# Kernel tuning notes

Hardware: AMD Instinct MI355X
Metric: run time of the kernel (lower is better)

The kernel has to match this reference:

```python
import jax, jax.numpy as jnp
import numpy as np

TOPK = 2
NUM_EXPERTS = 8

def setup_inputs() -> dict:
    key = jax.random.key(0)
    kx, kg, k1, k3, k2 = jax.random.split(key, 5)
    B, S, D, F, E = 1, 2048, 1024, 1024, NUM_EXPERTS
    x = jax.random.normal(kx, (B, S, D), dtype=jnp.float32)
    wg = jax.random.normal(kg, (E, D), dtype=jnp.float32) * (1.0 / np.sqrt(D))
    w1 = jax.random.normal(k1, (E, D, F), dtype=jnp.float32) * (1.0 / np.sqrt(D))
    w3 = jax.random.normal(k3, (E, D, F), dtype=jnp.float32) * (1.0 / np.sqrt(D))
    w2 = jax.random.normal(k2, (E, F, D), dtype=jnp.float32) * (1.0 / np.sqrt(F))
    return {"x": x, "wg": wg, "w1": w1, "w3": w3, "w2": w2}

def reference(x, wg, w1, w3, w2):
    # x: [B, S, D] -> tokens [N, D]
    D = x.shape[-1]
    E = wg.shape[0]
    xt = x.reshape(-1, D)
    # Gating: Linear(no bias) + softmax over experts
    logits = xt @ wg.T                      # [N, E]
    gates = jax.nn.softmax(logits, axis=-1)
    # Top-k selection, normalize weights (normalize_expert_weights=True),
    # routed_scaling_factor = 1.0
    weights, idx = jax.lax.top_k(gates, TOPK)      # [N, k]
    weights = weights / weights.sum(axis=-1, keepdims=True)
    # Per-token per-expert combine weight (dispatch+combine equivalent)
    comb = (jax.nn.one_hot(idx, E, dtype=xt.dtype) * weights[..., None]).sum(axis=1)  # [N, E]
    # SwiGLU experts (grouped GEMM equivalent, dense over experts)
    h = jnp.einsum('nd,edf->enf', xt, w1)   # gate proj
    u = jnp.einsum('nd,edf->enf', xt, w3)   # up proj
    a = jax.nn.silu(h) * u                  # [E, N, F]
    out = jnp.einsum('enf,efd,ne->nd', a, w2, comb)
    return out.reshape(x.shape), logits
```

## Files before the change

### kernel.cpp

```cpp
#include <hip/hip_runtime.h>
#include <stdint.h>

typedef unsigned short u16;
typedef __attribute__((ext_vector_type(8))) __bf16 bf16x8;
typedef __attribute__((ext_vector_type(4))) float f32x4;

#define MAXMT 40
#define N_TOK 2048
#define DDIM 1024
#define FDIM 1024

#define DEV static __device__ __forceinline__

DEV float bf2f(u16 u) {
    union { uint32_t i; float f; } v;
    v.i = ((uint32_t)u) << 16;
    return v.f;
}
DEV u16 f2bf(float f) {
    union { float f; uint32_t i; } v;
    v.f = f;
    uint32_t x = v.i;
    return (u16)((x + 0x7fffu + ((x >> 16) & 1u)) >> 16);
}

DEV void async_copy16(const u16* gsrc, u16* ldst) {
    __builtin_amdgcn_global_load_lds(
        (const __attribute__((address_space(1))) void*)(uintptr_t)gsrc,
        (__attribute__((address_space(3))) void*)(uint32_t)(uintptr_t)ldst,
        16, 0, 0);
}

DEV int sniff_fp(const void* p, int tid, int* scnt) {
    if (tid == 0) *scnt = 0;
    __syncthreads();
    u16 u = ((const u16*)p)[tid & 255];
    int e = (u >> 7) & 0xff;
    if (e != 0 && (e < 90 || e > 160)) atomicAdd(scnt, 1);
    __syncthreads();
    return *scnt > 64;
}

__global__ void k_mega(const void* __restrict__ x, const void* __restrict__ wg,
                       const void* __restrict__ w1, const void* __restrict__ w3,
                       const void* __restrict__ w2, u16* __restrict__ wt,
                       u16* __restrict__ xb, void* __restrict__ out_base,
                       int* __restrict__ te, float* __restrict__ tw) {
    __shared__ int scnt;
    __shared__ __align__(16) u16 s[64][72];
    int z = blockIdx.z, tid = threadIdx.x;

    if (z < 24) {
        int which = z >> 3, mat = z & 7;
        const void* src0 = which == 0 ? w1 : (which == 1 ? w3 : w2);
        int fp = sniff_fp(src0, tid, &scnt);
        u16* dst = wt + ((size_t)z) * 1048576;
        int r = tid >> 2, seg = tid & 3;
        int r0 = blockIdx.y * 64, c0 = blockIdx.x * 64;
        size_t base = (size_t)mat * 1048576 + (size_t)(r0 + r) * 1024 + c0 + seg * 16;
        u16 v[16];
        if (fp) {
            const float* sp = (const float*)src0 + base;
#pragma unroll
            for (int q = 0; q < 4; q++) {
                float4 f = ((const float4*)sp)[q];
                v[q * 4 + 0] = f2bf(f.x); v[q * 4 + 1] = f2bf(f.y);
                v[q * 4 + 2] = f2bf(f.z); v[q * 4 + 3] = f2bf(f.w);
            }
        } else {
            const u16* sp = (const u16*)src0 + base;
            *(uint4*)&v[0] = *(const uint4*)sp;
            *(uint4*)&v[8] = *(const uint4*)(sp + 8);
        }
        *(uint4*)&s[r][seg * 16] = *(const uint4*)&v[0];
        *(uint4*)&s[r][seg * 16 + 8] = *(const uint4*)&v[8];
        __syncthreads();
        int col = tid & 63, rgrp = tid >> 6;
        u16 tmp[16];
#pragma unroll
        for (int j = 0; j < 16; j++) tmp[j] = s[rgrp * 16 + j][col];
        u16* dp = dst + (size_t)(c0 + col) * 1024 + r0 + rgrp * 16;
        *(uint4*)dp = *(const uint4*)&tmp[0];
        *(uint4*)(dp + 8) = *(const uint4*)&tmp[8];
    } else {
        int fp = sniff_fp(x, tid, &scnt);
        int gi = (z - 24) * 256 + blockIdx.y * 16 + blockIdx.x;
        int wave = tid >> 6, lane = tid & 63;
        int n = gi * 4 + wave;
        float acc[8];
#pragma unroll
        for (int e = 0; e < 8; e++) acc[e] = 0.f;
        if (fp) {
            const float* xp = (const float*)x + (size_t)n * DDIM;
            const float* wp = (const float*)wg;
            for (int it = 0; it < 16; ++it) {
                int d = it * 64 + lane;
                float xv = xp[d];
                xb[(size_t)n * DDIM + d] = f2bf(xv);
#pragma unroll
                for (int e = 0; e < 8; e++) acc[e] += xv * wp[e * DDIM + d];
            }
        } else {
            const u16* xp = (const u16*)x + (size_t)n * DDIM;
            const u16* wp = (const u16*)wg;
            for (int it = 0; it < 16; ++it) {
                int d = it * 64 + lane;
                u16 raw = xp[d];
                xb[(size_t)n * DDIM + d] = raw;
                float xv = bf2f(raw);
#pragma unroll
                for (int e = 0; e < 8; e++) acc[e] += xv * bf2f(wp[e * DDIM + d]);
            }
        }
#pragma unroll
        for (int e = 0; e < 8; e++) {
            for (int off = 32; off; off >>= 1) acc[e] += __shfl_xor(acc[e], off);
        }
        if (lane < 8) {
            if (fp) ((float*)out_base + (size_t)N_TOK * DDIM)[n * 8 + lane] = acc[lane];
            else    ((u16*)out_base + (size_t)N_TOK * DDIM)[n * 8 + lane] = f2bf(acc[lane]);
        }
        if (lane == 0) {
            int e0 = 0; float b0 = acc[0];
            for (int e = 1; e < 8; e++) if (acc[e] > b0) { b0 = acc[e]; e0 = e; }
            int e1 = -1; float b1 = -1e30f;
            for (int e = 0; e < 8; e++) if (e != e0 && acc[e] > b1) { b1 = acc[e]; e1 = e; }
            float m = fmaxf(b0, b1);
            float x0 = __expf(b0 - m), x1 = __expf(b1 - m);
            float sden = x0 + x1;
            te[n * 2] = e0; te[n * 2 + 1] = e1;
            tw[n * 2] = x0 / sden; tw[n * 2 + 1] = x1 / sden;
        }
    }
}

__global__ void k_sched(const int* __restrict__ te, const float* __restrict__ tw,
                        int* __restrict__ pair_token, float* __restrict__ pair_weight,
                        int* __restrict__ sched) {
    __shared__ int cnt[8], cur[8];
    int t = threadIdx.x;
    if (t < 8) cnt[t] = 0;
    __syncthreads();
    for (int n = t; n < N_TOK; n += 256) {
        atomicAdd(&cnt[te[2 * n]], 1);
        atomicAdd(&cnt[te[2 * n + 1]], 1);
    }
    __syncthreads();
    if (t == 0) {
        int o = 0, mt = 0;
        for (int e = 0; e < 8; e++) {
            cur[e] = o;
            int c = cnt[e];
            for (int m0 = 0; m0 < c; m0 += 128) {
                sched[mt] = e;
                sched[MAXMT + mt] = o + m0;
                sched[2 * MAXMT + mt] = (c - m0 < 128) ? (c - m0) : 128;
                mt++;
            }
            o += c;
        }
        sched[3 * MAXMT] = mt;
        for (int i = mt; i < MAXMT; i++) { sched[i] = 0; sched[MAXMT + i] = 0; sched[2 * MAXMT + i] = 0; }
    }
    __syncthreads();
    for (int n = t; n < N_TOK; n += 256) {
#pragma unroll
        for (int s = 0; s < 2; s++) {
            int e = te[2 * n + s];
            int p = atomicAdd(&cur[e], 1);
            pair_token[p] = n;
            pair_weight[p] = tw[2 * n + s];
        }
    }
}

__launch_bounds__(256, 3)
__global__ void k_gemm13(const u16* __restrict__ xb, const u16* __restrict__ w1t,
                         const u16* __restrict__ w3t, const int* __restrict__ pair_token,
                         const int* __restrict__ sched, u16* __restrict__ Abuf) {
    __shared__ __align__(16) u16 smem[16384];
    u16* sA  = smem;
    u16* sB1 = smem + 8192;
    u16* sB3 = smem + 12288;

    int bn = blockIdx.x;
    int bm = blockIdx.y;
    int total = sched[3 * MAXMT];
    if (bm >= total) return;
    int e = sched[bm];
    int row0 = sched[MAXMT + bm];
    int rowsv = sched[2 * MAXMT + bm];

    int tid = threadIdx.x;
    int wave = tid >> 6, lane = tid & 63;
    int wm = wave & 1, wn = wave >> 1;
    int quad = lane >> 4, l15 = lane & 15;
    int lsub = lane >> 3, slot = lane & 7;

    const u16* gA[4]; u16* lA[4];
#pragma unroll
    for (int c = 0; c < 4; c++) {
        int row = c * 32 + wave * 8 + lsub;
        int cr = row < rowsv ? row : 0;
        int tok = pair_token[row0 + cr];
        int gch = slot ^ (row & 7);
        gA[c] = xb + (size_t)tok * DDIM + gch * 8;
        lA[c] = sA + c * 2048 + wave * 512;
    }
    const u16* gB1[2]; const u16* gB3[2]; int lBoff[2];
#pragma unroll
    for (int c = 0; c < 2; c++) {
        int row = c * 32 + wave * 8 + lsub;
        int gch = slot ^ (row & 7);
        int fcol = bn * 64 + row;
        gB1[c] = w1t + ((size_t)e * 1024 + fcol) * 1024 + gch * 8;
        gB3[c] = w3t + ((size_t)e * 1024 + fcol) * 1024 + gch * 8;
        lBoff[c] = c * 2048 + wave * 512;
    }

    f32x4 acc_h[4][2], acc_u[4][2];
#pragma unroll
    for (int i = 0; i < 4; i++)
#pragma unroll
        for (int j = 0; j < 2; j++) { acc_h[i][j] = (f32x4)0.f; acc_u[i][j] = (f32x4)0.f; }

    for (int kt = 0; kt < 16; ++kt) {
        int k0 = kt * 64;
        __syncthreads();
#pragma unroll
        for (int c = 0; c < 4; c++) async_copy16(gA[c] + k0, lA[c]);
#pragma unroll
        for (int c = 0; c < 2; c++) {
            async_copy16(gB1[c] + k0, sB1 + lBoff[c]);
            async_copy16(gB3[c] + k0, sB3 + lBoff[c]);
        }
        __syncthreads();
#pragma unroll
        for (int kk = 0; kk < 2; ++kk) {
            bf16x8 a[4], b1[2], b3[2];
#pragma unroll
            for (int i = 0; i < 4; i++) {
                int m = wm * 64 + i * 16 + l15;
                int s = (kk * 4 + quad) ^ (m & 7);
                a[i] = *(const bf16x8*)&sA[m * 64 + s * 8];
            }
#pragma unroll
            for (int j = 0; j < 2; j++) {
                int nn = wn * 32 + j * 16 + l15;
                int s = (kk * 4 + quad) ^ (nn & 7);
                b1[j] = *(const bf16x8*)&sB1[nn * 64 + s * 8];
                b3[j] = *(const bf16x8*)&sB3[nn * 64 + s * 8];
            }
#pragma unroll
            for (int i = 0; i < 4; i++)
#pragma unroll
                for (int j = 0; j < 2; j++) {
                    acc_h[i][j] = __builtin_amdgcn_mfma_f32_16x16x32_bf16(a[i], b1[j], acc_h[i][j], 0, 0, 0);
                    acc_u[i][j] = __builtin_amdgcn_mfma_f32_16x16x32_bf16(a[i], b3[j], acc_u[i][j], 0, 0, 0);
                }
        }
    }
    __syncthreads();
#pragma unroll
    for (int i = 0; i < 4; i++)
#pragma unroll
        for (int j = 0; j < 2; j++)
#pragma unroll
            for (int r = 0; r < 4; r++) {
                int row = wm * 64 + i * 16 + quad * 4 + r;
                int col = wn * 32 + j * 16 + l15;
                float h = acc_h[i][j][r], u = acc_u[i][j][r];
                smem[row * 72 + col] = f2bf(h * u / (1.0f + __expf(-h)));
            }
    __syncthreads();
    int rt = tid >> 1, half = tid & 1;
    if (rt < rowsv) {
        u16* dp = Abuf + (size_t)(row0 + rt) * FDIM + bn * 64 + half * 32;
        const u16* sp = &smem[rt * 72 + half * 32];
#pragma unroll
        for (int q = 0; q < 4; q++)
            *(uint4*)(dp + q * 8) = *(const uint4*)(sp + q * 8);
    }
}

__launch_bounds__(256, 3)
__global__ void k_gemm2(const u16* __restrict__ Abuf, const u16* __restrict__ w2t,
                        const int* __restrict__ pair_token, const float* __restrict__ pair_weight,
                        const int* __restrict__ sched, float* __restrict__ outf) {
    __shared__ __align__(16) u16 smem[12288];
    u16* sA = smem;
    u16* sB = smem + 8192;

    int bn = blockIdx.x;
    int bm = blockIdx.y;
    int total = sched[3 * MAXMT];
    if (bm >= total) return;
    int e = sched[bm];
    int row0 = sched[MAXMT + bm];
    int rowsv = sched[2 * MAXMT + bm];

    int tid = threadIdx.x;
    int wave = tid >> 6, lane = tid & 63;
    int wm = wave & 1, wn = wave >> 1;
    int quad = lane >> 4, l15 = lane & 15;
    int lsub = lane >> 3, slot = lane & 7;

    const u16* gA[4]; u16* lA[4];
#pragma unroll
    for (int c = 0; c < 4; c++) {
        int row = c * 32 + wave * 8 + lsub;
        int cr = row < rowsv ? row : 0;
        int gch = slot ^ (row & 7);
        gA[c] = Abuf + (size_t)(row0 + cr) * FDIM + gch * 8;
        lA[c] = sA + c * 2048 + wave * 512;
    }
    const u16* gB[2]; u16* lB[2];
#pragma unroll
    for (int c = 0; c < 2; c++) {
        int row = c * 32 + wave * 8 + lsub;
        int gch = slot ^ (row & 7);
        int dcol = bn * 64 + row;
        gB[c] = w2t + ((size_t)e * 1024 + dcol) * 1024 + gch * 8;
        lB[c] = sB + c * 2048 + wave * 512;
    }

    f32x4 acc[4][2];
#pragma unroll
    for (int i = 0; i < 4; i++)
#pragma unroll
        for (int j = 0; j < 2; j++) acc[i][j] = (f32x4)0.f;

    for (int kt = 0; kt < 16; ++kt) {
        int k0 = kt * 64;
        __syncthreads();
#pragma unroll
        for (int c = 0; c < 4; c++) async_copy16(gA[c] + k0, lA[c]);
#pragma unroll
        for (int c = 0; c < 2; c++) async_copy16(gB[c] + k0, lB[c]);
        __syncthreads();
#pragma unroll
        for (int kk = 0; kk < 2; ++kk) {
            bf16x8 a[4], b[2];
#pragma unroll
            for (int i = 0; i < 4; i++) {
                int m = wm * 64 + i * 16 + l15;
                int s = (kk * 4 + quad) ^ (m & 7);
                a[i] = *(const bf16x8*)&sA[m * 64 + s * 8];
            }
#pragma unroll
            for (int j = 0; j < 2; j++) {
                int nn = wn * 32 + j * 16 + l15;
                int s = (kk * 4 + quad) ^ (nn & 7);
                b[j] = *(const bf16x8*)&sB[nn * 64 + s * 8];
            }
#pragma unroll
            for (int i = 0; i < 4; i++)
#pragma unroll
                for (int j = 0; j < 2; j++)
                    acc[i][j] = __builtin_amdgcn_mfma_f32_16x16x32_bf16(a[i], b[j], acc[i][j], 0, 0, 0);
        }
    }
#pragma unroll
    for (int i = 0; i < 4; i++)
#pragma unroll
        for (int r = 0; r < 4; r++) {
            int lr = wm * 64 + i * 16 + quad * 4 + r;
            if (lr < rowsv) {
                int p = row0 + lr;
                int tok = pair_token[p];
                float w = pair_weight[p];
                float* op = outf + (size_t)tok * DDIM + bn * 64 + wn * 32 + l15;
#pragma unroll
                for (int j = 0; j < 2; j++)
                    atomicAdd(op + j * 16, w * acc[i][j][r]);
            }
        }
}

extern "C" void kernel_launch(void* const* d_in, const int* in_sizes, int n_in,
                              void* d_out, int out_size, void* d_ws, size_t ws_size,
                              hipStream_t stream) {
    const void* x  = d_in[0];
    const void* wg = d_in[1];
    const void* w1 = d_in[2];
    const void* w3 = d_in[3];
    const void* w2 = d_in[4];

    u16* wt   = (u16*)d_ws;
    u16* w1t  = wt;
    u16* w3t  = wt + (size_t)8 * 1048576;
    u16* w2t  = wt + (size_t)16 * 1048576;
    u16* Abuf = wt + (size_t)24 * 1048576;
    u16* xb   = Abuf + (size_t)4096 * 1024;
    int*   te   = (int*)(xb + (size_t)N_TOK * DDIM);
    float* tw   = (float*)(te + 2 * N_TOK);
    int*   ptok = (int*)(tw + 2 * N_TOK);
    float* pwt  = (float*)(ptok + 2 * N_TOK);
    int*   sched = (int*)(pwt + 2 * N_TOK);

    hipMemsetAsync(d_out, 0, (size_t)N_TOK * DDIM * sizeof(float), stream);
    k_mega<<<dim3(16, 16, 26), 256, 0, stream>>>(x, wg, w1, w3, w2, wt, xb, d_out, te, tw);
    k_sched<<<1, 256, 0, stream>>>(te, tw, ptok, pwt, sched);
    k_gemm13<<<dim3(16, MAXMT), 256, 0, stream>>>(xb, w1t, w3t, ptok, sched, Abuf);
    k_gemm2<<<dim3(16, MAXMT), 256, 0, stream>>>(Abuf, w2t, ptok, pwt, sched, (float*)d_out);
}
```

Before: 216.0 us.

## Enlarge transpose tiles, fold output zeroing into mega kernel, pad LDS

```diff
diff --git a/kernel.cpp b/kernel.cpp
--- a/kernel.cpp
+++ b/kernel.cpp
@@ -41,50 +41,76 @@
     return *scnt > 64;
 }
 
+__launch_bounds__(256, 4)
 __global__ void k_mega(const void* __restrict__ x, const void* __restrict__ wg,
                        const void* __restrict__ w1, const void* __restrict__ w3,
                        const void* __restrict__ w2, u16* __restrict__ wt,
                        u16* __restrict__ xb, void* __restrict__ out_base,
                        int* __restrict__ te, float* __restrict__ tw) {
     __shared__ int scnt;
-    __shared__ __align__(16) u16 s[64][72];
+    __shared__ __align__(16) u16 s[256 * 66];
     int z = blockIdx.z, tid = threadIdx.x;
 
     if (z < 24) {
         int which = z >> 3, mat = z & 7;
         const void* src0 = which == 0 ? w1 : (which == 1 ? w3 : w2);
         int fp = sniff_fp(src0, tid, &scnt);
-        u16* dst = wt + ((size_t)z) * 1048576;
-        int r = tid >> 2, seg = tid & 3;
-        int r0 = blockIdx.y * 64, c0 = blockIdx.x * 64;
-        size_t base = (size_t)mat * 1048576 + (size_t)(r0 + r) * 1024 + c0 + seg * 16;
-        u16 v[16];
+        u16* dst = wt + (size_t)z * 1048576;
+        int r0 = blockIdx.y * 256, c0 = blockIdx.x * 64;
+        int rsub = tid >> 2, seg = tid & 3;
+
+        union { u16 v[16]; uint32_t w32[8]; uint4 q4[2]; } buf[4];
         if (fp) {
-            const float* sp = (const float*)src0 + base;
-#pragma unroll
-            for (int q = 0; q < 4; q++) {
-                float4 f = ((const float4*)sp)[q];
-                v[q * 4 + 0] = f2bf(f.x); v[q * 4 + 1] = f2bf(f.y);
-                v[q * 4 + 2] = f2bf(f.z); v[q * 4 + 3] = f2bf(f.w);
-            }
+            const float* sp = (const float*)src0 + (size_t)mat * 1048576;
+            float4 ld[16];
+#pragma unroll
+            for (int it = 0; it < 4; ++it) {
+                int row = it * 64 + rsub;
+                const float4* p = (const float4*)(sp + (size_t)(r0 + row) * 1024 + c0 + seg * 16);
+#pragma unroll
+                for (int q = 0; q < 4; ++q) ld[it * 4 + q] = p[q];
+            }
+#pragma unroll
+            for (int it = 0; it < 4; ++it)
+#pragma unroll
+                for (int q = 0; q < 4; ++q) {
+                    float4 f = ld[it * 4 + q];
+                    buf[it].v[q * 4 + 0] = f2bf(f.x); buf[it].v[q * 4 + 1] = f2bf(f.y);
+                    buf[it].v[q * 4 + 2] = f2bf(f.z); buf[it].v[q * 4 + 3] = f2bf(f.w);
+                }
         } else {
-            const u16* sp = (const u16*)src0 + base;
-            *(uint4*)&v[0] = *(const uint4*)sp;
-            *(uint4*)&v[8] = *(const uint4*)(sp + 8);
-        }
-        *(uint4*)&s[r][seg * 16] = *(const uint4*)&v[0];
-        *(uint4*)&s[r][seg * 16 + 8] = *(const uint4*)&v[8];
+            const u16* sp = (const u16*)src0 + (size_t)mat * 1048576;
+#pragma unroll
+            for (int it = 0; it < 4; ++it) {
+                int row = it * 64 + rsub;
+                const uint4* p = (const uint4*)(sp + (size_t)(r0 + row) * 1024 + c0 + seg * 16);
+                buf[it].q4[0] = p[0];
+                buf[it].q4[1] = p[1];
+            }
+        }
+        uint32_t* sd = (uint32_t*)s;
+#pragma unroll
+        for (int it = 0; it < 4; ++it) {
+            int row = it * 64 + rsub;
+            int base = row * 33 + seg * 8;
+#pragma unroll
+            for (int q = 0; q < 8; ++q) sd[base + q] = buf[it].w32[q];
+        }
         __syncthreads();
-        int col = tid & 63, rgrp = tid >> 6;
-        u16 tmp[16];
-#pragma unroll
-        for (int j = 0; j < 16; j++) tmp[j] = s[rgrp * 16 + j][col];
-        u16* dp = dst + (size_t)(c0 + col) * 1024 + r0 + rgrp * 16;
-        *(uint4*)dp = *(const uint4*)&tmp[0];
-        *(uint4*)(dp + 8) = *(const uint4*)&tmp[8];
-    } else {
+        int d = tid >> 2, sub = tid & 3;
+#pragma unroll
+        for (int it = 0; it < 4; ++it) {
+            int j = it * 4 + sub;
+            u16 tmp[16];
+#pragma unroll
+            for (int i = 0; i < 16; ++i) tmp[i] = s[(j * 16 + i) * 66 + d];
+            u16* dp = dst + (size_t)(c0 + d) * 1024 + r0 + j * 16;
+            *(uint4*)dp = *(const uint4*)&tmp[0];
+            *(uint4*)(dp + 8) = *(const uint4*)&tmp[8];
+        }
+    } else if (z < 32) {
         int fp = sniff_fp(x, tid, &scnt);
-        int gi = (z - 24) * 256 + blockIdx.y * 16 + blockIdx.x;
+        int gi = (z - 24) * 64 + blockIdx.y * 16 + blockIdx.x;
         int wave = tid >> 6, lane = tid & 63;
         int n = gi * 4 + wave;
         float acc[8];
@@ -131,6 +157,11 @@
             te[n * 2] = e0; te[n * 2 + 1] = e1;
             tw[n * 2] = x0 / sden; tw[n * 2 + 1] = x1 / sden;
         }
+    } else {
+        float4* op = (float4*)out_base + ((size_t)(z - 32) * 64 + blockIdx.y * 16 + blockIdx.x) * 2048;
+        float4 zz = { 0.f, 0.f, 0.f, 0.f };
+#pragma unroll
+        for (int q = 0; q < 8; ++q) op[q * 256 + tid] = zz;
     }
 }
 
@@ -398,8 +429,7 @@
     float* pwt  = (float*)(ptok + 2 * N_TOK);
     int*   sched = (int*)(pwt + 2 * N_TOK);
 
-    hipMemsetAsync(d_out, 0, (size_t)N_TOK * DDIM * sizeof(float), stream);
-    k_mega<<<dim3(16, 16, 26), 256, 0, stream>>>(x, wg, w1, w3, w2, wt, xb, d_out, te, tw);
+    k_mega<<<dim3(16, 4, 36), 256, 0, stream>>>(x, wg, w1, w3, w2, wt, xb, d_out, te, tw);
     k_sched<<<1, 256, 0, stream>>>(te, tw, ptok, pwt, sched);
     k_gemm13<<<dim3(16, MAXMT), 256, 0, stream>>>(xb, w1t, w3t, ptok, sched, Abuf);
     k_gemm2<<<dim3(16, MAXMT), 256, 0, stream>>>(Abuf, w2t, ptok, pwt, sched, (float*)d_out);
```

Result: no change. 214.5 us (-0.7%).
